# Kernel tuning notes

Hardware: AMD Instinct MI355X
Metric: run time of the kernel (lower is better)

## Reference

```python
import jax, jax.numpy as jnp
import numpy as np

N_NODES = 100000
N_EDGES = 1200000
D = 64
E_CHARGE = np.float32(1.602176634e-19)   # elementary charge (fp32, like the torch buffer)
EPS0 = np.float32(8.8541878128e-12)      # vacuum permittivity (fp32 buffer)


def _mish(x):
    return x * jnp.tanh(jax.nn.softplus(x))


def _mlp(x, w1, b1, w2, b2):
    # nn.Linear convention: y = x @ W.T + b
    h = _mish(x @ w1.T + b1)
    return h @ w2.T + b2


def setup_inputs() -> dict:
    key = jax.random.key(0)
    ks = jax.random.split(key, 20)
    s = 1.0 / np.sqrt(D)
    inp = {
        "node_feats": jax.random.normal(ks[0], (N_NODES, D), jnp.float32),
        "edge_feats": jax.random.normal(ks[1], (N_EDGES, D), jnp.float32),
        "src": jax.random.randint(ks[2], (N_EDGES,), 0, N_NODES),
        "dst": jax.random.randint(ks[3], (N_EDGES,), 0, N_NODES),
    }
    names = ["ws", "wd", "we", "wm"]
    i = 4
    for nm in names:
        inp[nm + "_w1"] = jax.random.normal(ks[i], (D, D), jnp.float32) * s; i += 1
        inp[nm + "_b1"] = jax.random.normal(ks[i], (D,), jnp.float32) * s; i += 1
        inp[nm + "_w2"] = jax.random.normal(ks[i], (D, D), jnp.float32) * s; i += 1
        inp[nm + "_b2"] = jax.random.normal(ks[i], (D,), jnp.float32) * s; i += 1
    return inp


def reference(node_feats, edge_feats, src, dst,
              ws_w1, ws_b1, ws_w2, ws_b2,
              wd_w1, wd_b1, wd_w2, wd_b2,
              we_w1, we_b1, we_w2, we_b2,
              wm_w1, wm_b1, wm_w2, wm_b2):
    # node MLPs then per-edge gather
    h_src = _mlp(node_feats, ws_w1, ws_b1, ws_w2, ws_b2)[src]   # [E, D]
    h_dst = _mlp(node_feats, wd_w1, wd_b1, wd_w2, wd_b2)[dst]   # [E, D]
    ef = _mlp(edge_feats, we_w1, we_b1, we_w2, we_b2)            # [E, D]
    # h_nodes * e^2 / (4*pi*eps0 * edge * 1e-10), all in fp32 like torch
    num = h_src * h_dst * (E_CHARGE ** 2)
    den = np.float32(4.0 * np.pi) * EPS0 * ef * np.float32(1e-10)
    h_nodes = num / den                                          # [E, D]
    m = _mlp(h_nodes, wm_w1, wm_b1, wm_w2, wm_b2)                # [E, D]
    # scatter-sum messages into destination nodes
    h = jax.ops.segment_sum(m, dst, num_segments=N_NODES)        # [N, D]
    return jax.nn.softplus(node_feats + h)
```

## Files before the change

kernel.cpp:

```cpp
#include <hip/hip_runtime.h>
#include <math.h>

#define NNODES 100000
#define NEDGES 1200000

#define C_EC   1.602176634e-19f
#define C_E2   (C_EC * C_EC)
#define C_4PI  12.566370614359172f
#define C_EPS0 8.8541878128e-12f
#define C_A    (C_4PI * C_EPS0)
#define C_B    1e-10f

typedef __attribute__((ext_vector_type(8))) short bf16x8;
typedef __attribute__((ext_vector_type(4))) float f32x4;

__device__ __forceinline__ unsigned short f2bf(float f) {
    unsigned u = __float_as_uint(f);
    u += 0x7fffu + ((u >> 16) & 1u);
    return (unsigned short)(u >> 16);
}
__device__ __forceinline__ float bf2f(unsigned short s) {
    return __uint_as_float(((unsigned)s) << 16);
}
__device__ __forceinline__ float softplus_f(float x) {
    return fmaxf(x, 0.0f) + log1pf(__expf(-fabsf(x)));
}
__device__ __forceinline__ float mish_f(float x) {
    float e = __expf(fminf(x, 30.0f));
    float n = e * e + 2.0f * e;
    return x * n / (n + 2.0f);
}

__device__ __forceinline__ void mfma_layer(const unsigned short* xs,
                                           const unsigned short* __restrict__ wg,
                                           const float* __restrict__ bias,
                                           int lane, f32x4 acc[4])
{
    const int l15 = lane & 15, q = lane >> 4;
    bf16x8 a0 = *(const bf16x8*)(xs + l15 * 72 + q * 8);
    bf16x8 a1 = *(const bf16x8*)(xs + l15 * 72 + 32 + q * 8);
    #pragma unroll
    for (int t = 0; t < 4; ++t) {
        float bv = bias[t * 16 + l15];
        acc[t] = (f32x4){bv, bv, bv, bv};
        bf16x8 b0 = *(const bf16x8*)(wg + (t * 16 + l15) * 64 + q * 8);
        bf16x8 b1 = *(const bf16x8*)(wg + (t * 16 + l15) * 64 + 32 + q * 8);
        acc[t] = __builtin_amdgcn_mfma_f32_16x16x32_bf16(a0, b0, acc[t], 0, 0, 0);
        acc[t] = __builtin_amdgcn_mfma_f32_16x16x32_bf16(a1, b1, acc[t], 0, 0, 0);
    }
}

__device__ __forceinline__ void mish_to_lds(const f32x4 acc[4], unsigned short* hid, int lane)
{
    const int l15 = lane & 15, q = lane >> 4;
    #pragma unroll
    for (int t = 0; t < 4; ++t)
        #pragma unroll
        for (int j = 0; j < 4; ++j)
            hid[(q * 4 + j) * 72 + t * 16 + l15] = f2bf(mish_f(acc[t][j]));
}

__global__ __launch_bounds__(256) void convert_w_kernel(
    const float* __restrict__ w0, const float* __restrict__ w1,
    const float* __restrict__ w2, const float* __restrict__ w3,
    const float* __restrict__ w4, const float* __restrict__ w5,
    const float* __restrict__ w6, const float* __restrict__ w7,
    unsigned short* __restrict__ wbf)
{
    int g = blockIdx.x * 256 + threadIdx.x;
    int m = g >> 10;
    int e = (g & 1023) * 4;
    const float* w;
    switch (m) {
        case 0: w = w0; break; case 1: w = w1; break;
        case 2: w = w2; break; case 3: w = w3; break;
        case 4: w = w4; break; case 5: w = w5; break;
        case 6: w = w6; break; default: w = w7; break;
    }
    float4 v = *(const float4*)(w + e);
    unsigned short* dp = wbf + m * 4096 + e;
    dp[0] = f2bf(v.x); dp[1] = f2bf(v.y); dp[2] = f2bf(v.z); dp[3] = f2bf(v.w);
}

__global__ __launch_bounds__(256) void node_mlp_kernel(
    const float* __restrict__ x,
    const unsigned short* __restrict__ wbf,
    const float* __restrict__ bs1, const float* __restrict__ bs2,
    const float* __restrict__ bd1, const float* __restrict__ bd2,
    unsigned short* __restrict__ hs, unsigned short* __restrict__ hd)
{
    __shared__ __align__(16) unsigned short xs[64 * 72];
    __shared__ __align__(16) unsigned short hid[64 * 72];
    const int t = threadIdx.x, lane = t & 63, wave = t >> 6;
    const int row0 = blockIdx.x * 64 + wave * 16;
    unsigned short* xw = xs + wave * 16 * 72;
    unsigned short* hw = hid + wave * 16 * 72;
    const int l15 = lane & 15, q = lane >> 4;

    {
        int r = lane >> 2, c4 = lane & 3;
        #pragma unroll
        for (int i = 0; i < 4; ++i) {
            int col = (c4 + i * 4) * 4;
            float4 v = make_float4(0.f, 0.f, 0.f, 0.f);
            if (row0 + r < NNODES) v = *(const float4*)(x + (size_t)(row0 + r) * 64 + col);
            unsigned short* dp = xw + r * 72 + col;
            dp[0] = f2bf(v.x); dp[1] = f2bf(v.y); dp[2] = f2bf(v.z); dp[3] = f2bf(v.w);
        }
    }
    __syncthreads();

    f32x4 acc[4];
    mfma_layer(xw, wbf + 0 * 4096, bs1, lane, acc);
    mish_to_lds(acc, hw, lane);
    __syncthreads();
    mfma_layer(hw, wbf + 1 * 4096, bs2, lane, acc);
    #pragma unroll
    for (int j = 0; j < 4; ++j) {
        int row = row0 + q * 4 + j;
        if (row < NNODES)
            #pragma unroll
            for (int t4 = 0; t4 < 4; ++t4)
                hs[(size_t)row * 64 + t4 * 16 + l15] = f2bf(acc[t4][j]);
    }
    mfma_layer(xw, wbf + 2 * 4096, bd1, lane, acc);
    __syncthreads();
    mish_to_lds(acc, hw, lane);
    __syncthreads();
    mfma_layer(hw, wbf + 3 * 4096, bd2, lane, acc);
    #pragma unroll
    for (int j = 0; j < 4; ++j) {
        int row = row0 + q * 4 + j;
        if (row < NNODES)
            #pragma unroll
            for (int t4 = 0; t4 < 4; ++t4)
                hd[(size_t)row * 64 + t4 * 16 + l15] = f2bf(acc[t4][j]);
    }
}

__global__ __launch_bounds__(256) void edge_kernel(
    const float* __restrict__ efeat,
    const unsigned short* __restrict__ hs, const unsigned short* __restrict__ hd,
    const int* __restrict__ src, const int* __restrict__ dst,
    const unsigned short* __restrict__ wbf,
    const float* __restrict__ be1, const float* __restrict__ be2,
    const float* __restrict__ bm1, const float* __restrict__ bm2,
    float* __restrict__ out)
{
    __shared__ __align__(16) unsigned short xs[64 * 72];
    __shared__ __align__(16) unsigned short hid[64 * 72];
    const int t = threadIdx.x, lane = t & 63, wave = t >> 6;
    const int e0 = blockIdx.x * 64 + wave * 16;
    unsigned short* xw = xs + wave * 16 * 72;
    unsigned short* hw = hid + wave * 16 * 72;
    const int l15 = lane & 15, q = lane >> 4;

    {
        int r = lane >> 2, c4 = lane & 3;
        #pragma unroll
        for (int i = 0; i < 4; ++i) {
            int col = (c4 + i * 4) * 4;
            float4 v = *(const float4*)(efeat + (size_t)(e0 + r) * 64 + col);
            unsigned short* dp = xw + r * 72 + col;
            dp[0] = f2bf(v.x); dp[1] = f2bf(v.y); dp[2] = f2bf(v.z); dp[3] = f2bf(v.w);
        }
    }
    int sj[4], dj[4];
    #pragma unroll
    for (int j = 0; j < 4; ++j) {
        sj[j] = src[e0 + q * 4 + j];
        dj[j] = dst[e0 + q * 4 + j];
    }
    __syncthreads();

    f32x4 acc[4], ef[4];
    mfma_layer(xw, wbf + 4 * 4096, be1, lane, acc);
    mish_to_lds(acc, hw, lane);
    __syncthreads();
    mfma_layer(hw, wbf + 5 * 4096, be2, lane, ef);
    __syncthreads();

    #pragma unroll
    for (int j = 0; j < 4; ++j)
        #pragma unroll
        for (int t4 = 0; t4 < 4; ++t4) {
            int col = t4 * 16 + l15;
            float a = bf2f(hs[(size_t)sj[j] * 64 + col]);
            float b = bf2f(hd[(size_t)dj[j] * 64 + col]);
            float den = (C_A * ef[t4][j]) * C_B;
            float h = (den != 0.0f) ? ((a * b) * C_E2) / den : 0.0f;
            h = fminf(fmaxf(h, -1e30f), 1e30f);
            xw[(q * 4 + j) * 72 + col] = f2bf(h);
        }
    __syncthreads();

    mfma_layer(xw, wbf + 6 * 4096, bm1, lane, acc);
    mish_to_lds(acc, hw, lane);
    __syncthreads();
    mfma_layer(hw, wbf + 7 * 4096, bm2, lane, acc);

    #pragma unroll
    for (int j = 0; j < 4; ++j) {
        float* p = out + (size_t)dj[j] * 64;
        #pragma unroll
        for (int t4 = 0; t4 < 4; ++t4)
            atomicAdd(p + t4 * 16 + l15, acc[t4][j]);
    }
}

__global__ __launch_bounds__(256) void finalize_kernel(
    const float* __restrict__ nf, float* __restrict__ out)
{
    int g = blockIdx.x * 256 + threadIdx.x;
    float4 a = ((const float4*)nf)[g];
    float4 h = ((float4*)out)[g];
    float4 o;
    o.x = softplus_f(a.x + h.x);
    o.y = softplus_f(a.y + h.y);
    o.z = softplus_f(a.z + h.z);
    o.w = softplus_f(a.w + h.w);
    ((float4*)out)[g] = o;
}

extern "C" void kernel_launch(void* const* d_in, const int* in_sizes, int n_in,
                              void* d_out, int out_size, void* d_ws, size_t ws_size,
                              hipStream_t stream)
{
    const float* node_feats = (const float*)d_in[0];
    const float* edge_feats = (const float*)d_in[1];
    const int*   src        = (const int*)d_in[2];
    const int*   dst        = (const int*)d_in[3];
    const float* ws_w1 = (const float*)d_in[4];
    const float* ws_b1 = (const float*)d_in[5];
    const float* ws_w2 = (const float*)d_in[6];
    const float* ws_b2 = (const float*)d_in[7];
    const float* wd_w1 = (const float*)d_in[8];
    const float* wd_b1 = (const float*)d_in[9];
    const float* wd_w2 = (const float*)d_in[10];
    const float* wd_b2 = (const float*)d_in[11];
    const float* we_w1 = (const float*)d_in[12];
    const float* we_b1 = (const float*)d_in[13];
    const float* we_w2 = (const float*)d_in[14];
    const float* we_b2 = (const float*)d_in[15];
    const float* wm_w1 = (const float*)d_in[16];
    const float* wm_b1 = (const float*)d_in[17];
    const float* wm_w2 = (const float*)d_in[18];
    const float* wm_b2 = (const float*)d_in[19];

    unsigned short* wbf = (unsigned short*)d_ws;
    unsigned short* hs  = wbf + 8 * 4096;
    unsigned short* hd  = hs + (size_t)NNODES * 64;

    convert_w_kernel<<<32, 256, 0, stream>>>(
        ws_w1, ws_w2, wd_w1, wd_w2, we_w1, we_w2, wm_w1, wm_w2, wbf);

    node_mlp_kernel<<<(NNODES + 63) / 64, 256, 0, stream>>>(
        node_feats, wbf, ws_b1, ws_b2, wd_b1, wd_b2, hs, hd);

    hipMemsetAsync(d_out, 0, (size_t)out_size * sizeof(float), stream);

    edge_kernel<<<NEDGES / 64, 256, 0, stream>>>(
        edge_feats, hs, hd, src, dst, wbf, we_b1, we_b2, wm_b1, wm_b2, (float*)d_out);

    finalize_kernel<<<(NNODES * 64) / (256 * 4), 256, 0, stream>>>(
        node_feats, (float*)d_out);
}
```

Baseline: 840.2 us.

## Permute hidden K layout for vector LDS/global access and use wave-level sync

Weights for second-layer and message MLPs are stored with a permuted K ordering. This lets each lane write its four MFMA output columns as a single 8-byte vector to LDS and to the hs/hd buffers, and lets the edge kernel gather hs/hd rows with vector loads issued early. Block-wide __syncthreads are replaced with wavefront barriers, since each wave only touches its own LDS rows. Divisions in mish and in the Coulomb term now use a fast reciprocal, and the output memset is folded into the node MLP kernel. The cost is extra layout complexity and slightly less precise reciprocal arithmetic.

```diff
diff --git a/kernel.cpp b/kernel.cpp
--- a/kernel.cpp
+++ b/kernel.cpp
@@ -13,6 +13,12 @@
 
 typedef __attribute__((ext_vector_type(8))) short bf16x8;
 typedef __attribute__((ext_vector_type(4))) float f32x4;
+typedef __attribute__((ext_vector_type(4))) unsigned short u16x4;
+
+__device__ __forceinline__ void wave_sync() {
+    __builtin_amdgcn_fence(__ATOMIC_ACQ_REL, "wavefront");
+    __builtin_amdgcn_wave_barrier();
+}
 
 __device__ __forceinline__ unsigned short f2bf(float f) {
     unsigned u = __float_as_uint(f);
@@ -28,8 +34,9 @@
 __device__ __forceinline__ float mish_f(float x) {
     float e = __expf(fminf(x, 30.0f));
     float n = e * e + 2.0f * e;
-    return x * n / (n + 2.0f);
-}
+    return x * n * __builtin_amdgcn_rcpf(n + 2.0f);
+}
+
 
 __device__ __forceinline__ void mfma_layer(const unsigned short* xs,
                                            const unsigned short* __restrict__ wg,
@@ -50,14 +57,18 @@
     }
 }
 
-__device__ __forceinline__ void mish_to_lds(const f32x4 acc[4], unsigned short* hid, int lane)
+__device__ __forceinline__ void mish_to_lds_perm(const f32x4 acc[4], unsigned short* hid, int lane)
 {
     const int l15 = lane & 15, q = lane >> 4;
     #pragma unroll
-    for (int t = 0; t < 4; ++t)
-        #pragma unroll
-        for (int j = 0; j < 4; ++j)
-            hid[(q * 4 + j) * 72 + t * 16 + l15] = f2bf(mish_f(acc[t][j]));
+    for (int j = 0; j < 4; ++j) {
+        u16x4 v;
+        v[0] = f2bf(mish_f(acc[0][j]));
+        v[1] = f2bf(mish_f(acc[1][j]));
+        v[2] = f2bf(mish_f(acc[2][j]));
+        v[3] = f2bf(mish_f(acc[3][j]));
+        *(u16x4*)(hid + (q * 4 + j) * 72 + l15 * 4) = v;
+    }
 }
 
 __global__ __launch_bounds__(256) void convert_w_kernel(
@@ -78,8 +89,12 @@
         case 6: w = w6; break; default: w = w7; break;
     }
     float4 v = *(const float4*)(w + e);
-    unsigned short* dp = wbf + m * 4096 + e;
-    dp[0] = f2bf(v.x); dp[1] = f2bf(v.y); dp[2] = f2bf(v.z); dp[3] = f2bf(v.w);
+    int n = e >> 6, k = e & 63;
+    bool perm = (m == 1) || (m == 3) || (m >= 5);
+    int kk = perm ? ((k & 15) * 4 + (k >> 4)) : k;
+    int st = perm ? 4 : 1;
+    unsigned short* dp = wbf + m * 4096 + n * 64 + kk;
+    dp[0] = f2bf(v.x); dp[st] = f2bf(v.y); dp[2 * st] = f2bf(v.z); dp[3 * st] = f2bf(v.w);
 }
 
 __global__ __launch_bounds__(256) void node_mlp_kernel(
@@ -87,7 +102,8 @@
     const unsigned short* __restrict__ wbf,
     const float* __restrict__ bs1, const float* __restrict__ bs2,
     const float* __restrict__ bd1, const float* __restrict__ bd2,
-    unsigned short* __restrict__ hs, unsigned short* __restrict__ hd)
+    unsigned short* __restrict__ hs, unsigned short* __restrict__ hd,
+    float* __restrict__ out)
 {
     __shared__ __align__(16) unsigned short xs[64 * 72];
     __shared__ __align__(16) unsigned short hid[64 * 72];
@@ -96,6 +112,16 @@
     unsigned short* xw = xs + wave * 16 * 72;
     unsigned short* hw = hid + wave * 16 * 72;
     const int l15 = lane & 15, q = lane >> 4;
+
+    {
+        int r = lane >> 2, c4 = lane & 3;
+        if (row0 + r < NNODES) {
+            float4 z = make_float4(0.f, 0.f, 0.f, 0.f);
+            #pragma unroll
+            for (int i = 0; i < 4; ++i)
+                *(float4*)(out + (size_t)(row0 + r) * 64 + (c4 + i * 4) * 4) = z;
+        }
+    }
 
     {
         int r = lane >> 2, c4 = lane & 3;
@@ -108,33 +134,38 @@
             dp[0] = f2bf(v.x); dp[1] = f2bf(v.y); dp[2] = f2bf(v.z); dp[3] = f2bf(v.w);
         }
     }
-    __syncthreads();
+    wave_sync();
 
     f32x4 acc[4];
     mfma_layer(xw, wbf + 0 * 4096, bs1, lane, acc);
-    mish_to_lds(acc, hw, lane);
-    __syncthreads();
+    wave_sync();
+    mish_to_lds_perm(acc, hw, lane);
+    wave_sync();
     mfma_layer(hw, wbf + 1 * 4096, bs2, lane, acc);
     #pragma unroll
     for (int j = 0; j < 4; ++j) {
         int row = row0 + q * 4 + j;
-        if (row < NNODES)
-            #pragma unroll
-            for (int t4 = 0; t4 < 4; ++t4)
-                hs[(size_t)row * 64 + t4 * 16 + l15] = f2bf(acc[t4][j]);
+        if (row < NNODES) {
+            u16x4 v;
+            v[0] = f2bf(acc[0][j]); v[1] = f2bf(acc[1][j]);
+            v[2] = f2bf(acc[2][j]); v[3] = f2bf(acc[3][j]);
+            *(u16x4*)(hs + (size_t)row * 64 + l15 * 4) = v;
+        }
     }
     mfma_layer(xw, wbf + 2 * 4096, bd1, lane, acc);
-    __syncthreads();
-    mish_to_lds(acc, hw, lane);
-    __syncthreads();
+    wave_sync();
+    mish_to_lds_perm(acc, hw, lane);
+    wave_sync();
     mfma_layer(hw, wbf + 3 * 4096, bd2, lane, acc);
     #pragma unroll
     for (int j = 0; j < 4; ++j) {
         int row = row0 + q * 4 + j;
-        if (row < NNODES)
-            #pragma unroll
-            for (int t4 = 0; t4 < 4; ++t4)
-                hd[(size_t)row * 64 + t4 * 16 + l15] = f2bf(acc[t4][j]);
+        if (row < NNODES) {
+            u16x4 v;
+            v[0] = f2bf(acc[0][j]); v[1] = f2bf(acc[1][j]);
+            v[2] = f2bf(acc[2][j]); v[3] = f2bf(acc[3][j]);
+            *(u16x4*)(hd + (size_t)row * 64 + l15 * 4) = v;
+        }
     }
 }
 
@@ -171,32 +202,43 @@
         sj[j] = src[e0 + q * 4 + j];
         dj[j] = dst[e0 + q * 4 + j];
     }
-    __syncthreads();
+    u16x4 va[4], vb[4];
+    #pragma unroll
+    for (int j = 0; j < 4; ++j) {
+        va[j] = *(const u16x4*)(hs + (size_t)sj[j] * 64 + l15 * 4);
+        vb[j] = *(const u16x4*)(hd + (size_t)dj[j] * 64 + l15 * 4);
+    }
+    wave_sync();
 
     f32x4 acc[4], ef[4];
     mfma_layer(xw, wbf + 4 * 4096, be1, lane, acc);
-    mish_to_lds(acc, hw, lane);
-    __syncthreads();
+    wave_sync();
+    mish_to_lds_perm(acc, hw, lane);
+    wave_sync();
     mfma_layer(hw, wbf + 5 * 4096, be2, lane, ef);
-    __syncthreads();
-
-    #pragma unroll
-    for (int j = 0; j < 4; ++j)
+    wave_sync();
+
+    #pragma unroll
+    for (int j = 0; j < 4; ++j) {
+        u16x4 hv;
         #pragma unroll
         for (int t4 = 0; t4 < 4; ++t4) {
-            int col = t4 * 16 + l15;
-            float a = bf2f(hs[(size_t)sj[j] * 64 + col]);
-            float b = bf2f(hd[(size_t)dj[j] * 64 + col]);
+            float a = bf2f(va[j][t4]);
+            float b = bf2f(vb[j][t4]);
             float den = (C_A * ef[t4][j]) * C_B;
-            float h = (den != 0.0f) ? ((a * b) * C_E2) / den : 0.0f;
+            float num = (a * b) * C_E2;
+            float h = (den != 0.0f) ? num * __builtin_amdgcn_rcpf(den) : 0.0f;
             h = fminf(fmaxf(h, -1e30f), 1e30f);
-            xw[(q * 4 + j) * 72 + col] = f2bf(h);
-        }
-    __syncthreads();
+            hv[t4] = f2bf(h);
+        }
+        *(u16x4*)(xw + (q * 4 + j) * 72 + l15 * 4) = hv;
+    }
+    wave_sync();
 
     mfma_layer(xw, wbf + 6 * 4096, bm1, lane, acc);
-    mish_to_lds(acc, hw, lane);
-    __syncthreads();
+    wave_sync();
+    mish_to_lds_perm(acc, hw, lane);
+    wave_sync();
     mfma_layer(hw, wbf + 7 * 4096, bm2, lane, acc);
 
     #pragma unroll
@@ -255,9 +297,7 @@
         ws_w1, ws_w2, wd_w1, wd_w2, we_w1, we_w2, wm_w1, wm_w2, wbf);
 
     node_mlp_kernel<<<(NNODES + 63) / 64, 256, 0, stream>>>(
-        node_feats, wbf, ws_b1, ws_b2, wd_b1, wd_b2, hs, hd);
-
-    hipMemsetAsync(d_out, 0, (size_t)out_size * sizeof(float), stream);
+        node_feats, wbf, ws_b1, ws_b2, wd_b1, wd_b2, hs, hd, (float*)d_out);
 
     edge_kernel<<<NEDGES / 64, 256, 0, stream>>>(
         edge_feats, hs, hd, src, dst, wbf, we_b1, we_b2, wm_b1, wm_b2, (float*)d_out);
```

Result: faster. 781.9 us (-6.9%).
